# Kernel optimization log

Hardware: AMD Instinct MI355X
Metric: run time of the kernel (lower is better)

The kernel has to match this reference:

```python
import jax, jax.numpy as jnp
import numpy as np

NUM_CLASSES = 5  # sleep stages: W, N1, N2, N3, REM
N = 4194304


def setup_inputs() -> dict:
    key = jax.random.key(0)
    k1, k2 = jax.random.split(key)
    inputs = jax.random.normal(k1, (N, NUM_CLASSES), dtype=jnp.float32)
    targets = jax.random.randint(k2, (N,), 0, NUM_CLASSES, dtype=jnp.int32)
    return {"inputs": inputs, "targets": targets}


def reference(inputs, targets):
    # Mean False Error loss: per-class mean of per-sample cross-entropy,
    # summed over classes that are present in the batch.
    # per-sample CE loss (stable log-softmax, single pass)
    logp = jax.nn.log_softmax(inputs, axis=-1)                    # [N, C]
    per_sample = -jnp.take_along_axis(logp, targets[:, None].astype(jnp.int32), axis=1)[:, 0]  # [N]
    # segment-reduce by class label (replaces the python grouping loop)
    loss_sums = jax.ops.segment_sum(per_sample, targets, num_segments=NUM_CLASSES)             # [C]
    counts = jax.ops.segment_sum(jnp.ones_like(per_sample), targets, num_segments=NUM_CLASSES) # [C]
    # per-class mean; empty classes contribute 0
    means = jnp.where(counts > 0, loss_sums / jnp.maximum(counts, 1.0), 0.0)
    return jnp.sum(means)
```

## Files before the change

kernel.cpp:

```cpp
#include <hip/hip_runtime.h>

#define NCLS 5
#define NSAMP 4194304
#define BLOCK 256
#define GRID (NSAMP / 4 / BLOCK)

__device__ __forceinline__ void accum_sample(float l0, float l1, float l2, float l3, float l4,
                                             int t, float sums[NCLS], float cnts[NCLS]) {
    float m = fmaxf(fmaxf(fmaxf(l0, l1), fmaxf(l2, l3)), l4);
    float s = __expf(l0 - m) + __expf(l1 - m) + __expf(l2 - m) +
              __expf(l3 - m) + __expf(l4 - m);
    float lt = (t == 0) ? l0 : (t == 1) ? l1 : (t == 2) ? l2 : (t == 3) ? l3 : l4;
    float ce = __logf(s) + m - lt;
#pragma unroll
    for (int k = 0; k < NCLS; ++k) {
        bool hit = (t == k);
        sums[k] += hit ? ce : 0.0f;
        cnts[k] += hit ? 1.0f : 0.0f;
    }
}

__global__ __launch_bounds__(BLOCK) void mfe_partial(const float* __restrict__ inputs,
                                                     const int* __restrict__ targets,
                                                     float* __restrict__ acc ) {
    const int tid = blockIdx.x * BLOCK + threadIdx.x;
    const int base = tid * 4;

    const float4* in4 = (const float4*)(inputs + (size_t)base * NCLS);
    float4 a = in4[0];
    float4 b = in4[1];
    float4 c = in4[2];
    float4 d = in4[3];
    float4 e = in4[4];
    int4 t4 = *(const int4*)(targets + base);

    float sums[NCLS] = {0.f, 0.f, 0.f, 0.f, 0.f};
    float cnts[NCLS] = {0.f, 0.f, 0.f, 0.f, 0.f};

    accum_sample(a.x, a.y, a.z, a.w, b.x, t4.x, sums, cnts);
    accum_sample(b.y, b.z, b.w, c.x, c.y, t4.y, sums, cnts);
    accum_sample(c.z, c.w, d.x, d.y, d.z, t4.z, sums, cnts);
    accum_sample(d.w, e.x, e.y, e.z, e.w, t4.w, sums, cnts);

#pragma unroll
    for (int k = 0; k < NCLS; ++k) {
#pragma unroll
        for (int off = 32; off > 0; off >>= 1) {
            sums[k] += __shfl_down(sums[k], off, 64);
            cnts[k] += __shfl_down(cnts[k], off, 64);
        }
    }

    __shared__ float ls[BLOCK / 64][2 * NCLS];
    const int lane = threadIdx.x & 63;
    const int wave = threadIdx.x >> 6;
    if (lane == 0) {
#pragma unroll
        for (int k = 0; k < NCLS; ++k) {
            ls[wave][k] = sums[k];
            ls[wave][NCLS + k] = cnts[k];
        }
    }
    __syncthreads();

    if (threadIdx.x < 2 * NCLS) {
        float v = 0.f;
#pragma unroll
        for (int w = 0; w < BLOCK / 64; ++w) v += ls[w][threadIdx.x];
        atomicAdd(acc + threadIdx.x, v);
    }
}

__global__ void mfe_final(const float* __restrict__ acc, float* __restrict__ out) {
    if (threadIdx.x == 0 && blockIdx.x == 0) {
        float total = 0.f;
#pragma unroll
        for (int k = 0; k < NCLS; ++k) {
            float cnt = acc[NCLS + k];
            if (cnt > 0.f) total += acc[k] / cnt;
        }
        out[0] = total;
    }
}

extern "C" void kernel_launch(void* const* d_in, const int* in_sizes, int n_in,
                              void* d_out, int out_size, void* d_ws, size_t ws_size,
                              hipStream_t stream) {
    const float* inputs = (const float*)d_in[0];
    const int* targets = (const int*)d_in[1];
    float* out = (float*)d_out;
    float* acc = (float*)d_ws;

    hipMemsetAsync(acc, 0, 2 * NCLS * sizeof(float), stream);

    mfe_partial<<<GRID, BLOCK, 0, stream>>>(inputs, targets, acc);
    mfe_final<<<1, 64, 0, stream>>>(acc, out);
}
```

Baseline: 167.7 us.

## Replace global atomics with per-block partials and two-stage reduction

```diff
diff --git a/kernel.cpp b/kernel.cpp
--- a/kernel.cpp
+++ b/kernel.cpp
@@ -3,7 +3,10 @@
 #define NCLS 5
 #define NSAMP 4194304
 #define BLOCK 256
-#define GRID (NSAMP / 4 / BLOCK)
+#define GRID 1024
+#define NTHREADS (GRID * BLOCK)
+#define ITERS (NSAMP / (NTHREADS * 4))
+#define NVALS (2 * NCLS)
 
 __device__ __forceinline__ void accum_sample(float l0, float l1, float l2, float l3, float l4,
                                              int t, float sums[NCLS], float cnts[NCLS]) {
@@ -20,28 +23,8 @@
     }
 }
 
-__global__ __launch_bounds__(BLOCK) void mfe_partial(const float* __restrict__ inputs,
-                                                     const int* __restrict__ targets,
-                                                     float* __restrict__ acc ) {
-    const int tid = blockIdx.x * BLOCK + threadIdx.x;
-    const int base = tid * 4;
-
-    const float4* in4 = (const float4*)(inputs + (size_t)base * NCLS);
-    float4 a = in4[0];
-    float4 b = in4[1];
-    float4 c = in4[2];
-    float4 d = in4[3];
-    float4 e = in4[4];
-    int4 t4 = *(const int4*)(targets + base);
-
-    float sums[NCLS] = {0.f, 0.f, 0.f, 0.f, 0.f};
-    float cnts[NCLS] = {0.f, 0.f, 0.f, 0.f, 0.f};
-
-    accum_sample(a.x, a.y, a.z, a.w, b.x, t4.x, sums, cnts);
-    accum_sample(b.y, b.z, b.w, c.x, c.y, t4.y, sums, cnts);
-    accum_sample(c.z, c.w, d.x, d.y, d.z, t4.z, sums, cnts);
-    accum_sample(d.w, e.x, e.y, e.z, e.w, t4.w, sums, cnts);
-
+__device__ __forceinline__ void block_reduce_10(float sums[NCLS], float cnts[NCLS],
+                                                float* result10 ) {
 #pragma unroll
     for (int k = 0; k < NCLS; ++k) {
 #pragma unroll
@@ -50,8 +33,7 @@
             cnts[k] += __shfl_down(cnts[k], off, 64);
         }
     }
-
-    __shared__ float ls[BLOCK / 64][2 * NCLS];
+    __shared__ float ls[BLOCK / 64][NVALS];
     const int lane = threadIdx.x & 63;
     const int wave = threadIdx.x >> 6;
     if (lane == 0) {
@@ -62,24 +44,77 @@
         }
     }
     __syncthreads();
-
-    if (threadIdx.x < 2 * NCLS) {
+    if (threadIdx.x < NVALS) {
         float v = 0.f;
 #pragma unroll
         for (int w = 0; w < BLOCK / 64; ++w) v += ls[w][threadIdx.x];
-        atomicAdd(acc + threadIdx.x, v);
+        *result10 = v;
     }
 }
 
-__global__ void mfe_final(const float* __restrict__ acc, float* __restrict__ out) {
-    if (threadIdx.x == 0 && blockIdx.x == 0) {
-        float total = 0.f;
+__global__ __launch_bounds__(BLOCK) void mfe_partial(const float* __restrict__ inputs,
+                                                     const int* __restrict__ targets,
+                                                     float* __restrict__ partial ) {
+    const int tid = blockIdx.x * BLOCK + threadIdx.x;
+
+    float sums[NCLS] = {0.f, 0.f, 0.f, 0.f, 0.f};
+    float cnts[NCLS] = {0.f, 0.f, 0.f, 0.f, 0.f};
+
+#pragma unroll
+    for (int it = 0; it < ITERS; ++it) {
+        const int chunk = it * NTHREADS + tid;
+        const int base = chunk * 4;
+        const float4* in4 = (const float4*)(inputs + (size_t)base * NCLS);
+        float4 a = in4[0];
+        float4 b = in4[1];
+        float4 c = in4[2];
+        float4 d = in4[3];
+        float4 e = in4[4];
+        int4 t4 = *(const int4*)(targets + base);
+
+        accum_sample(a.x, a.y, a.z, a.w, b.x, t4.x, sums, cnts);
+        accum_sample(b.y, b.z, b.w, c.x, c.y, t4.y, sums, cnts);
+        accum_sample(c.z, c.w, d.x, d.y, d.z, t4.z, sums, cnts);
+        accum_sample(d.w, e.x, e.y, e.z, e.w, t4.w, sums, cnts);
+    }
+
+    float total;
+    block_reduce_10(sums, cnts, &total);
+    if (threadIdx.x < NVALS) {
+        partial[threadIdx.x * GRID + blockIdx.x] = total;
+    }
+}
+
+__global__ __launch_bounds__(BLOCK) void mfe_final(const float* __restrict__ partial,
+                                                   float* __restrict__ out) {
+    float sums[NCLS];
+    float cnts[NCLS];
+#pragma unroll
+    for (int k = 0; k < NCLS; ++k) {
+        float s = 0.f, c = 0.f;
+#pragma unroll
+        for (int i = 0; i < GRID / BLOCK; ++i) {
+            s += partial[k * GRID + threadIdx.x + i * BLOCK];
+            c += partial[(NCLS + k) * GRID + threadIdx.x + i * BLOCK];
+        }
+        sums[k] = s;
+        cnts[k] = c;
+    }
+
+    float total;
+    block_reduce_10(sums, cnts, &total);
+
+    __shared__ float fin[NVALS];
+    if (threadIdx.x < NVALS) fin[threadIdx.x] = total;
+    __syncthreads();
+    if (threadIdx.x == 0) {
+        float loss = 0.f;
 #pragma unroll
         for (int k = 0; k < NCLS; ++k) {
-            float cnt = acc[NCLS + k];
-            if (cnt > 0.f) total += acc[k] / cnt;
+            float cnt = fin[NCLS + k];
+            if (cnt > 0.f) loss += fin[k] / cnt;
         }
-        out[0] = total;
+        out[0] = loss;
     }
 }
 
@@ -89,10 +124,8 @@
     const float* inputs = (const float*)d_in[0];
     const int* targets = (const int*)d_in[1];
     float* out = (float*)d_out;
-    float* acc = (float*)d_ws;
+    float* partial = (float*)d_ws;
 
-    hipMemsetAsync(acc, 0, 2 * NCLS * sizeof(float), stream);
-
-    mfe_partial<<<GRID, BLOCK, 0, stream>>>(inputs, targets, acc);
-    mfe_final<<<1, 64, 0, stream>>>(acc, out);
+    mfe_partial<<<GRID, BLOCK, 0, stream>>>(inputs, targets, partial);
+    mfe_final<<<1, BLOCK, 0, stream>>>(partial, out);
 }
```

Result: faster. 137.5 us (-18.0%).
